# Performance work log

Measured on AMD Instinct MI355X. Metric: run time of the kernel, lower is better.

Reference implementation:

```python
import jax, jax.numpy as jnp
import numpy as np
from jax import lax

CC = 0.25       # commitment cost
EPS_GN = 1e-5   # GroupNorm eps (torch default)


def _conv(x, w, b=None, stride=1, pad=0):
    # x: [B, C, L], w: [O, I, K]
    y = lax.conv_general_dilated(x, w, (stride,), [(pad, pad)],
                                 dimension_numbers=('NCH', 'OIH', 'NCH'))
    if b is not None:
        y = y + b[None, :, None]
    return y


def _convT(x, w, b, pad_lo, pad_hi):
    # stride-2 ConvTranspose1d expressed as lhs-dilated conv; weights kept in
    # equivalent OIW conv form (pad = (k-1-p, k-1-p+output_padding))
    y = lax.conv_general_dilated(x, w, (1,), [(pad_lo, pad_hi)], lhs_dilation=(2,),
                                 dimension_numbers=('NCH', 'OIH', 'NCH'))
    return y + b[None, :, None]


def _gn(x, g, b, groups=8):
    B, C, L = x.shape
    xr = x.reshape(B, groups, C // groups, L)
    m = xr.mean(axis=(2, 3), keepdims=True)
    v = ((xr - m) ** 2).mean(axis=(2, 3), keepdims=True)
    xn = ((xr - m) * lax.rsqrt(v + EPS_GN)).reshape(B, C, L)
    return xn * g[None, :, None] + b[None, :, None]


def _res_block(x, gn1_g, gn1_b, c1_w, gn2_g, gn2_b, c2_w):
    h = jax.nn.relu(_gn(x, gn1_g, gn1_b))
    h = _conv(h, c1_w, None, 1, 1)
    h = jax.nn.relu(_gn(h, gn2_g, gn2_b))
    h = _conv(h, c2_w, None, 1, 0)
    return x + h


def _vq(z, codebook):
    # z: [B, D, L] -> [B, L, D]; eval-mode VQ (no EMA update)
    zin = jnp.transpose(z, (0, 2, 1))
    B, L, D = zin.shape
    flat = zin.reshape(-1, D)
    d = (flat ** 2).sum(1, keepdims=True) + (codebook ** 2).sum(1) - 2.0 * (flat @ codebook.T)
    idx = jnp.argmin(d, axis=1)                       # [B*L]
    q = codebook[idx].reshape(B, L, D)                # gather == onehot @ codebook
    loss = CC * jnp.mean((lax.stop_gradient(q) - zin) ** 2)
    q_st = zin + lax.stop_gradient(q - zin)           # straight-through
    enc = jax.nn.one_hot(idx, codebook.shape[0], dtype=z.dtype)  # [B*L, K]
    avg = enc.mean(0)
    perp = jnp.exp(-jnp.sum(avg * jnp.log(avg + 1e-10)))
    return loss, jnp.transpose(q_st, (0, 2, 1)), perp, enc


def _forward(x, e1_w, e1_b, e2_w, e2_b, e3_w, e3_b,
             r0_gn1_g, r0_gn1_b, r0_c1_w, r0_gn2_g, r0_gn2_b, r0_c2_w,
             r1_gn1_g, r1_gn1_b, r1_c1_w, r1_gn2_g, r1_gn2_b, r1_c2_w,
             pv_w, pv_b, codebook,
             d1_w, d1_b, d2_w, d2_b, d3_w, d3_b,
             bh1_w, bh1_b, bh2_w, bh2_b, bh3_w, bh3_b):
    # encoder: T -> T/4
    h = jax.nn.relu(_conv(x, e1_w, e1_b, 1, 3))
    h = jax.nn.relu(_conv(h, e2_w, e2_b, 2, 2))
    h = _conv(h, e3_w, e3_b, 2, 1)
    h = _res_block(h, r0_gn1_g, r0_gn1_b, r0_c1_w, r0_gn2_g, r0_gn2_b, r0_c2_w)
    h = _res_block(h, r1_gn1_g, r1_gn1_b, r1_c1_w, r1_gn2_g, r1_gn2_b, r1_c2_w)
    z = _conv(h, pv_w, pv_b, 1, 0)  # pre-VQ 1x1 conv; Dropout1d is identity in eval
    loss, quantized, perp, enc = _vq(z, codebook)
    # decoder: T/4 -> T (shapes match exactly; interpolate branches are no-ops)
    d = jax.nn.relu(_convT(quantized, d1_w, d1_b, 1, 2))  # k3 s2 p1 op1
    d = jax.nn.relu(_convT(d, d2_w, d2_b, 2, 3))          # k5 s2 p2 op1
    x_recon = _conv(d, d3_w, d3_b, 1, 3)                  # k7 p3
    z_pooled = quantized.mean(axis=2)                     # [B, D]
    beh = jax.nn.relu(z_pooled @ bh1_w.T + bh1_b)
    beh = jax.nn.relu(beh @ bh2_w.T + bh2_b)              # Dropout eval = identity
    beh = beh @ bh3_w.T + bh3_b
    return loss, x_recon, perp, quantized, enc, beh


def setup_inputs() -> dict:
    key = jax.random.key(0)
    ks = iter(jax.random.split(key, 48))
    def nrm(shape, std=1.0):
        return (std * jax.random.normal(next(ks), shape)).astype(jnp.float32)
    H, RH, D, K, N = 512, 128, 128, 1024, 128
    B, T = 32, 4096
    p = {}
    p['x'] = nrm((B, N, T))
    p['e1_w'] = nrm((H // 4, N, 7), (N * 7) ** -0.5); p['e1_b'] = jnp.zeros((H // 4,), jnp.float32)
    p['e2_w'] = nrm((H // 2, H // 4, 5), (H // 4 * 5) ** -0.5); p['e2_b'] = jnp.zeros((H // 2,), jnp.float32)
    p['e3_w'] = nrm((H, H // 2, 3), (H // 2 * 3) ** -0.5); p['e3_b'] = jnp.zeros((H,), jnp.float32)
    for r in range(2):
        p[f'r{r}_gn1_g'] = jnp.ones((H,), jnp.float32); p[f'r{r}_gn1_b'] = jnp.zeros((H,), jnp.float32)
        p[f'r{r}_c1_w'] = nrm((RH, H, 3), (H * 3) ** -0.5)
        p[f'r{r}_gn2_g'] = jnp.ones((RH,), jnp.float32); p[f'r{r}_gn2_b'] = jnp.zeros((RH,), jnp.float32)
        p[f'r{r}_c2_w'] = nrm((H, RH, 1), RH ** -0.5)
    p['pv_w'] = nrm((D, H, 1), H ** -0.5); p['pv_b'] = jnp.zeros((D,), jnp.float32)
    p['codebook'] = nrm((K, D))  # embedding.weight.data.normal_()
    p['d1_w'] = nrm((H, D, 3), (D * 3) ** -0.5); p['d1_b'] = jnp.zeros((H,), jnp.float32)
    p['d2_w'] = nrm((H // 2, H, 5), (H * 5) ** -0.5); p['d2_b'] = jnp.zeros((H // 2,), jnp.float32)
    p['d3_w'] = nrm((N, H // 2, 7), (H // 2 * 7) ** -0.5); p['d3_b'] = jnp.zeros((N,), jnp.float32)
    p['bh1_w'] = nrm((128, D), D ** -0.5); p['bh1_b'] = jnp.zeros((128,), jnp.float32)
    p['bh2_w'] = nrm((64, 128), 128 ** -0.5); p['bh2_b'] = jnp.zeros((64,), jnp.float32)
    p['bh3_w'] = nrm((4, 64), 64 ** -0.5); p['bh3_b'] = jnp.zeros((4,), jnp.float32)
    return p


def reference(x, e1_w, e1_b, e2_w, e2_b, e3_w, e3_b,
              r0_gn1_g, r0_gn1_b, r0_c1_w, r0_gn2_g, r0_gn2_b, r0_c2_w,
              r1_gn1_g, r1_gn1_b, r1_c1_w, r1_gn2_g, r1_gn2_b, r1_c2_w,
              pv_w, pv_b, codebook,
              d1_w, d1_b, d2_w, d2_b, d3_w, d3_b,
              bh1_w, bh1_b, bh2_w, bh2_b, bh3_w, bh3_b):
    return _forward(x, e1_w, e1_b, e2_w, e2_b, e3_w, e3_b,
                    r0_gn1_g, r0_gn1_b, r0_c1_w, r0_gn2_g, r0_gn2_b, r0_c2_w,
                    r1_gn1_g, r1_gn1_b, r1_c1_w, r1_gn2_g, r1_gn2_b, r1_c2_w,
                    pv_w, pv_b, codebook,
                    d1_w, d1_b, d2_w, d2_b, d3_w, d3_b,
                    bh1_w, bh1_b, bh2_w, bh2_b, bh3_w, bh3_b)
```

## Files before the change

### kernel.cpp

```cpp
#include <hip/hip_runtime.h>


#define SWZ32(j) ((j) + ((((j) >> 5)) << 2))

template<int K, int S, int TT, bool GN, bool RESID, bool RELU_OUT, bool TSTORE, bool VSTORE>
__global__ __launch_bounds__(256, 4) void convtile_k(
    const float* __restrict__ in, const float* __restrict__ w,
    const float* __restrict__ bias, float* __restrict__ out,
    const float* __restrict__ scale, const float* __restrict__ shift,
    const float* __restrict__ resid,
    int Cin, int Lin, int Lout, int pad, int Cout)
{
    constexpr int CI    = (K == 1) ? 32 : 16;
    constexpr int BT    = 16 * TT;
    constexpr int SPAN  = (BT - 1) * S + K;
    constexpr int WN    = (TT - 1) * S + K;
    constexpr int NW4   = (WN + 3) / 4;
    constexpr int JMAX  = 15 * TT * S + 4 * (NW4 - 1);
    constexpr int END1  = SWZ32(JMAX) + 4;
    constexpr int END2  = SWZ32(SPAN - 1) + 1;
    constexpr int SPANP = (((END1 > END2 ? END1 : END2) + 3) & ~3);
    constexpr int LWP   = 68;
    constexpr int PER   = (CI / 4) * K;
    constexpr int NQ    = TT / 4;

    __shared__ float lin[CI * SPANP];
    __shared__ float lw[CI * K * LWP];

    const int tid = threadIdx.x;
    const int tx = tid & 15, ty = tid >> 4;
    const int t0 = blockIdx.x * BT;
    const int o0 = blockIdx.y * 64;
    const int b  = blockIdx.z;

    float acc[4][TT];
    #pragma unroll
    for (int c = 0; c < 4; ++c) {
        float bv = bias ? bias[o0 + 4 * ty + c] : 0.0f;
        #pragma unroll
        for (int u = 0; u < TT; ++u) acc[c][u] = bv;
    }

    int off4[NW4];
    #pragma unroll
    for (int q = 0; q < NW4; ++q) {
        int j = TT * S * tx + 4 * q;
        off4[q] = SWZ32(j);
    }

    const float* inb = in + (size_t)b * Cin * Lin;
    const int p0 = t0 * S - pad;

    constexpr int TPR = 256 / CI;
    const int sci = tid / TPR, sj0 = tid % TPR;
    const int wco = tid >> 2, wpart = tid & 3;
    const int cibase = wpart * (CI / 4);

    for (int ci0 = 0; ci0 < Cin; ci0 += CI) {
        __syncthreads();
        {
            const float* srow = inb + (size_t)(ci0 + sci) * Lin;
            float sc = 0.f, sh = 0.f;
            if (GN) {
                sc = scale[b * Cin + ci0 + sci];
                sh = shift[b * Cin + ci0 + sci];
            }
            for (int j = sj0; j < SPAN; j += TPR) {
                int p = p0 + j;
                bool ok = (p >= 0) && (p < Lin);
                float v = ok ? srow[p] : 0.0f;
                if (GN) v = ok ? fmaxf(v * sc + sh, 0.0f) : 0.0f;
                lin[sci * SPANP + SWZ32(j)] = v;
            }
        }
        {
            const float* wsrc = w + (size_t)(o0 + wco) * Cin * K
                                  + (size_t)ci0 * K + wpart * PER;
            #pragma unroll
            for (int e = 0; e < PER / 4; ++e) {
                const float4 v = *(const float4*)(wsrc + 4 * e);
                #pragma unroll
                for (int i = 0; i < 4; ++i) {
                    const int rem = 4 * e + i;
                    const int cio = rem / K, kk = rem % K;
                    lw[((cibase + cio) * K + kk) * LWP + wco] = ((const float*)&v)[i];
                }
            }
        }
        __syncthreads();

        for (int ci = 0; ci < CI; ++ci) {
            float win[NW4 * 4];
            const float* lrow = &lin[ci * SPANP];
            #pragma unroll
            for (int q = 0; q < NW4; ++q)
                *(float4*)&win[4 * q] = *(const float4*)(lrow + off4[q]);
            #pragma unroll
            for (int k = 0; k < K; ++k) {
                const float4 wv = *(const float4*)&lw[(ci * K + k) * LWP + 4 * ty];
                #pragma unroll
                for (int u = 0; u < TT; ++u) {
                    float x = win[u * S + k];
                    acc[0][u] += x * wv.x;
                    acc[1][u] += x * wv.y;
                    acc[2][u] += x * wv.z;
                    acc[3][u] += x * wv.w;
                }
            }
        }
    }

    if (RESID) {
        #pragma unroll
        for (int c = 0; c < 4; ++c)
            #pragma unroll
            for (int q = 0; q < NQ; ++q) {
                const float4 rv = *(const float4*)(resid +
                    ((size_t)b * Cout + o0 + 4 * ty + c) * Lout + t0 + TT * tx + 4 * q);
                acc[c][4*q+0] += rv.x; acc[c][4*q+1] += rv.y;
                acc[c][4*q+2] += rv.z; acc[c][4*q+3] += rv.w;
            }
    }
    if (RELU_OUT) {
        #pragma unroll
        for (int c = 0; c < 4; ++c)
            #pragma unroll
            for (int u = 0; u < TT; ++u) acc[c][u] = fmaxf(acc[c][u], 0.f);
    }
    if (TSTORE) {
        #pragma unroll
        for (int u = 0; u < TT; ++u) {
            float4 v; v.x = acc[0][u]; v.y = acc[1][u]; v.z = acc[2][u]; v.w = acc[3][u];
            *(float4*)(out + ((size_t)b * Lout + t0 + TT * tx + u) * Cout + o0 + 4 * ty) = v;
        }
    } else if (VSTORE) {
        #pragma unroll
        for (int c = 0; c < 4; ++c)
            #pragma unroll
            for (int q = 0; q < NQ; ++q) {
                float4 v;
                v.x = acc[c][4*q+0]; v.y = acc[c][4*q+1];
                v.z = acc[c][4*q+2]; v.w = acc[c][4*q+3];
                *(float4*)(out + ((size_t)b * Cout + o0 + 4 * ty + c) * Lout
                           + t0 + TT * tx + 4 * q) = v;
            }
    } else {
        #pragma unroll
        for (int c = 0; c < 4; ++c)
            #pragma unroll
            for (int u = 0; u < TT; ++u)
                out[((size_t)b * Cout + o0 + 4 * ty + c) * Lout + t0 + TT * tx + u] = acc[c][u];
    }
}

template<int K, int TT>
__global__ __launch_bounds__(256, 4) void convttile_k(
    const float* __restrict__ in, const float* __restrict__ w,
    const float* __restrict__ bias, float* __restrict__ out,
    int Cin, int Lin, int Cout)
{
    constexpr int CI    = 16;
    constexpr int BT    = 16 * TT;
    constexpr int HALO  = (K == 5) ? 2 : 1;
    constexpr int SPAN  = BT + HALO;
    constexpr int WNl   = TT + HALO;
    constexpr int NW4   = (WNl + 3) / 4;
    constexpr int JMAX  = 15 * TT + 4 * (NW4 - 1);
    constexpr int END1  = SWZ32(JMAX) + 4;
    constexpr int END2  = SWZ32(SPAN - 1) + 1;
    constexpr int SPANP = (((END1 > END2 ? END1 : END2) + 3) & ~3);
    constexpr int LWP   = 68;
    constexpr int PER   = (CI / 4) * K;

    __shared__ float lin[CI * SPANP];
    __shared__ float lw[CI * K * LWP];

    const int tid = threadIdx.x;
    const int tx = tid & 15, ty = tid >> 4;
    const int t20 = blockIdx.x * BT;
    const int o0  = blockIdx.y * 64;
    const int b   = blockIdx.z;
    const int Lout = 2 * Lin;

    float accE[4][TT], accO[4][TT];
    #pragma unroll
    for (int c = 0; c < 4; ++c) {
        float bv = bias[o0 + 4 * ty + c];
        #pragma unroll
        for (int u = 0; u < TT; ++u) { accE[c][u] = bv; accO[c][u] = bv; }
    }

    int off4[NW4];
    #pragma unroll
    for (int q = 0; q < NW4; ++q) {
        int j = TT * tx + 4 * q;
        off4[q] = SWZ32(j);
    }

    const float* inb = in + (size_t)b * Cin * Lin;
    const int p0 = (K == 5) ? (t20 - 1) : t20;

    constexpr int TPR = 256 / CI;
    const int sci = tid / TPR, sj0 = tid % TPR;
    const int wco = tid >> 2, wpart = tid & 3;
    const int cibase = wpart * (CI / 4);

    for (int ci0 = 0; ci0 < Cin; ci0 += CI) {
        __syncthreads();
        {
            const float* srow = inb + (size_t)(ci0 + sci) * Lin;
            for (int j = sj0; j < SPAN; j += TPR) {
                int p = p0 + j;
                bool ok = (p >= 0) && (p < Lin);
                lin[sci * SPANP + SWZ32(j)] = ok ? srow[p] : 0.0f;
            }
        }
        {
            const float* wsrc = w + (size_t)(o0 + wco) * Cin * K
                                  + (size_t)ci0 * K + wpart * PER;
            #pragma unroll
            for (int e = 0; e < PER / 4; ++e) {
                const float4 v = *(const float4*)(wsrc + 4 * e);
                #pragma unroll
                for (int i = 0; i < 4; ++i) {
                    const int rem = 4 * e + i;
                    const int cio = rem / K, kk = rem % K;
                    lw[((cibase + cio) * K + kk) * LWP + wco] = ((const float*)&v)[i];
                }
            }
        }
        __syncthreads();

        for (int ci = 0; ci < CI; ++ci) {
            float win[NW4 * 4];
            const float* lrow = &lin[ci * SPANP];
            #pragma unroll
            for (int q = 0; q < NW4; ++q)
                *(float4*)&win[4 * q] = *(const float4*)(lrow + off4[q]);
            #pragma unroll
            for (int k = 0; k < K; ++k) {
                const float4 wv = *(const float4*)&lw[(ci * K + k) * LWP + 4 * ty];
                const int  joff = (K == 5) ? ((k + 1) >> 1) : (k >> 1);
                const bool toE  = (K == 5) ? ((k & 1) == 0) : (k == 1);
                #pragma unroll
                for (int u = 0; u < TT; ++u) {
                    float x = win[u + joff];
                    if (toE) {
                        accE[0][u] += x * wv.x;
                        accE[1][u] += x * wv.y;
                        accE[2][u] += x * wv.z;
                        accE[3][u] += x * wv.w;
                    } else {
                        accO[0][u] += x * wv.x;
                        accO[1][u] += x * wv.y;
                        accO[2][u] += x * wv.z;
                        accO[3][u] += x * wv.w;
                    }
                }
            }
        }
    }

    size_t base = ((size_t)b * Cout + o0 + 4 * ty) * (size_t)Lout + (size_t)(2 * (t20 + TT * tx));
    #pragma unroll
    for (int c = 0; c < 4; ++c) {
        #pragma unroll
        for (int q = 0; q < TT / 2; ++q) {
            float4 v;
            v.x = fmaxf(accE[c][2*q],   0.f); v.y = fmaxf(accO[c][2*q],   0.f);
            v.z = fmaxf(accE[c][2*q+1], 0.f); v.w = fmaxf(accO[c][2*q+1], 0.f);
            *(float4*)(out + base + (size_t)c * Lout + 4 * q) = v;
        }
    }
}

__global__ __launch_bounds__(256) void gnstats_k(
    const float* __restrict__ x, const float* __restrict__ g,
    const float* __restrict__ be, float* __restrict__ scale,
    float* __restrict__ shift, int C, int L, int G)
{
    int tid = threadIdx.x;
    int b = blockIdx.x / G, gr = blockIdx.x % G;
    int cpg = C / G;
    size_t n = (size_t)cpg * L;
    const float* base = x + ((size_t)b * C + (size_t)gr * cpg) * L;
    float s = 0.f, s2 = 0.f;
    for (size_t idx = tid; idx < n; idx += 256) { float v = base[idx]; s += v; s2 += v * v; }
    __shared__ float rs[256], rq[256];
    rs[tid] = s; rq[tid] = s2; __syncthreads();
    for (int off = 128; off > 0; off >>= 1) {
        if (tid < off) { rs[tid] += rs[tid + off]; rq[tid] += rq[tid + off]; }
        __syncthreads();
    }
    float mean = rs[0] / (float)n;
    float var  = rq[0] / (float)n - mean * mean;
    float inv  = rsqrtf(var + 1e-5f);
    if (tid < cpg) {
        int c = gr * cpg + tid;
        float ga = g[c], bb = be[c];
        scale[b * C + c] = inv * ga;
        shift[b * C + c] = bb - mean * inv * ga;
    }
}

__global__ __launch_bounds__(256) void vq_k(
    const float* __restrict__ z,
    const float* __restrict__ cb,
    float* __restrict__ out_q,
    float* __restrict__ lossAcc,
    unsigned int* __restrict__ hist,
    int* __restrict__ ip_out)
{
    const int tid = threadIdx.x;
    const int pbase = blockIdx.x * 64;
    __shared__ float zs[64 * 129];
    __shared__ float cbs[64 * 129];
    __shared__ float cn[64];
    __shared__ float rd[256];
    __shared__ int   ri[256];
    __shared__ int   ip[64];

    for (int f = tid; f < 64 * 128; f += 256) {
        int p = f >> 7, d = f & 127;
        zs[p * 129 + d] = z[(size_t)pbase * 128 + f];
    }

    float mind[4]; int minc[4];
    #pragma unroll
    for (int a = 0; a < 4; ++a) { mind[a] = 3.4e38f; minc[a] = 0; }
    const int tp = tid >> 4, tr = tid & 15;
    const int prow = tp * 4, crow = tr * 4;

    for (int ct = 0; ct < 16; ++ct) {
        __syncthreads();
        for (int f = tid; f < 64 * 128; f += 256) {
            int c = f >> 7, d = f & 127;
            cbs[c * 129 + d] = cb[((size_t)ct * 64 + c) * 128 + d];
        }
        __syncthreads();
        if (tid < 64) {
            float s = 0.f;
            for (int d = 0; d < 128; ++d) { float v = cbs[tid * 129 + d]; s += v * v; }
            cn[tid] = s;
        }
        __syncthreads();
        float dot[4][4];
        #pragma unroll
        for (int a = 0; a < 4; ++a)
            #pragma unroll
            for (int e = 0; e < 4; ++e) dot[a][e] = 0.f;
        for (int d = 0; d < 128; ++d) {
            float za[4], cc[4];
            #pragma unroll
            for (int a = 0; a < 4; ++a) za[a] = zs[(prow + a) * 129 + d];
            #pragma unroll
            for (int e = 0; e < 4; ++e) cc[e] = cbs[(crow + e) * 129 + d];
            #pragma unroll
            for (int a = 0; a < 4; ++a)
                #pragma unroll
                for (int e = 0; e < 4; ++e) dot[a][e] += za[a] * cc[e];
        }
        #pragma unroll
        for (int e = 0; e < 4; ++e) {
            int c = ct * 64 + crow + e;
            float cne = cn[crow + e];
            #pragma unroll
            for (int a = 0; a < 4; ++a) {
                float dist = cne - 2.0f * dot[a][e];
                if (dist < mind[a]) { mind[a] = dist; minc[a] = c; }
            }
        }
    }

    for (int a = 0; a < 4; ++a) {
        __syncthreads();
        rd[tid] = mind[a]; ri[tid] = minc[a];
        __syncthreads();
        if (tr == 0) {
            float bd = rd[tid]; int bi = ri[tid];
            for (int u = 1; u < 16; ++u) {
                float dv = rd[tid + u]; int iv = ri[tid + u];
                if (dv < bd || (dv == bd && iv < bi)) { bd = dv; bi = iv; }
            }
            ip[prow + a] = bi;
            atomicAdd(&hist[bi], 1u);
        }
    }
    __syncthreads();

    if (tid < 64) ip_out[pbase + tid] = ip[tid];

    float lp = 0.f;
    for (int f = tid; f < 64 * 128; f += 256) {
        int p = f >> 7, d = f & 127;
        int gp = pbase + p, b = gp >> 10, l = gp & 1023;
        float qv = cb[(size_t)ip[p] * 128 + d];
        float zv = zs[p * 129 + d];
        float df = qv - zv; lp += df * df;
        out_q[(((size_t)b * 128 + d) << 10) + l] = qv;
    }
    rd[tid] = lp; __syncthreads();
    for (int off = 128; off > 0; off >>= 1) {
        if (tid < off) rd[tid] += rd[tid + off];
        __syncthreads();
    }
    if (tid == 0) atomicAdd(lossAcc, rd[0]);
}

__global__ __launch_bounds__(256) void enc_k(
    const int* __restrict__ ip, float2* __restrict__ enc)
{
    size_t idx = (size_t)blockIdx.x * 256 + threadIdx.x;
    int p  = (int)(idx >> 9);
    int q2 = (int)(idx & 511);
    int best = ip[p];
    int c0 = q2 * 2;
    float2 v;
    v.x = (c0     == best) ? 1.0f : 0.0f;
    v.y = (c0 + 1 == best) ? 1.0f : 0.0f;
    enc[idx] = v;
}

__global__ __launch_bounds__(256) void pool_k(const float* __restrict__ q, float* __restrict__ zp)
{
    int tid = threadIdx.x;
    const float* row = q + (size_t)blockIdx.x * 1024;
    float s = 0.f;
    for (int l = tid; l < 1024; l += 256) s += row[l];
    __shared__ float rs[256];
    rs[tid] = s; __syncthreads();
    for (int off = 128; off > 0; off >>= 1) {
        if (tid < off) rs[tid] += rs[tid + off];
        __syncthreads();
    }
    if (tid == 0) zp[blockIdx.x] = rs[0] * (1.0f / 1024.0f);
}

__global__ __launch_bounds__(256) void beh_k(
    const float* __restrict__ zp,
    const float* __restrict__ w1, const float* __restrict__ b1,
    const float* __restrict__ w2, const float* __restrict__ b2,
    const float* __restrict__ w3, const float* __restrict__ b3,
    float* __restrict__ out)
{
    __shared__ float zs[32 * 128];
    __shared__ float h1s[32 * 128];
    __shared__ float h2s[32 * 64];
    int tid = threadIdx.x;
    for (int f = tid; f < 4096; f += 256) zs[f] = zp[f];
    __syncthreads();
    for (int f = tid; f < 4096; f += 256) {
        int bi = f >> 7, j = f & 127;
        float acc = b1[j];
        for (int d = 0; d < 128; ++d) acc += zs[bi * 128 + d] * w1[j * 128 + d];
        h1s[f] = fmaxf(acc, 0.f);
    }
    __syncthreads();
    for (int f = tid; f < 2048; f += 256) {
        int bi = f >> 6, j = f & 63;
        float acc = b2[j];
        for (int d = 0; d < 128; ++d) acc += h1s[bi * 128 + d] * w2[j * 128 + d];
        h2s[f] = fmaxf(acc, 0.f);
    }
    __syncthreads();
    if (tid < 128) {
        int bi = tid >> 2, j = tid & 3;
        float acc = b3[j];
        for (int d = 0; d < 64; ++d) acc += h2s[bi * 64 + d] * w3[j * 64 + d];
        out[tid] = acc;
    }
}

__global__ __launch_bounds__(1024) void init_k(unsigned int* hist, float* lossAcc)
{
    hist[threadIdx.x] = 0u;
    if (threadIdx.x == 0) *lossAcc = 0.f;
}

__global__ __launch_bounds__(1024) void fin_k(
    const unsigned int* __restrict__ hist, const float* __restrict__ lossAcc,
    float* __restrict__ out_loss, float* __restrict__ out_perp)
{
    __shared__ float rs[1024];
    int tid = threadIdx.x;
    float avg = (float)hist[tid] * (1.0f / 32768.0f);
    rs[tid] = avg * logf(avg + 1e-10f);
    __syncthreads();
    for (int off = 512; off > 0; off >>= 1) {
        if (tid < off) rs[tid] += rs[tid + off];
        __syncthreads();
    }
    if (tid == 0) {
        out_perp[0] = expf(-rs[0]);
        out_loss[0] = 0.25f * lossAcc[0] * (1.0f / 4194304.0f);
    }
}

extern "C" void kernel_launch(void* const* d_in, const int* in_sizes, int n_in,
                              void* d_out, int out_size, void* d_ws, size_t ws_size,
                              hipStream_t stream)
{
    const float* X    = (const float*)d_in[0];
    const float* e1w  = (const float*)d_in[1];  const float* e1b = (const float*)d_in[2];
    const float* e2w  = (const float*)d_in[3];  const float* e2b = (const float*)d_in[4];
    const float* e3w  = (const float*)d_in[5];  const float* e3b = (const float*)d_in[6];
    const float* r0g1g = (const float*)d_in[7];  const float* r0g1b = (const float*)d_in[8];
    const float* r0c1w = (const float*)d_in[9];
    const float* r0g2g = (const float*)d_in[10]; const float* r0g2b = (const float*)d_in[11];
    const float* r0c2w = (const float*)d_in[12];
    const float* r1g1g = (const float*)d_in[13]; const float* r1g1b = (const float*)d_in[14];
    const float* r1c1w = (const float*)d_in[15];
    const float* r1g2g = (const float*)d_in[16]; const float* r1g2b = (const float*)d_in[17];
    const float* r1c2w = (const float*)d_in[18];
    const float* pvw  = (const float*)d_in[19]; const float* pvb = (const float*)d_in[20];
    const float* CB   = (const float*)d_in[21];
    const float* d1w  = (const float*)d_in[22]; const float* d1b = (const float*)d_in[23];
    const float* d2w  = (const float*)d_in[24]; const float* d2b = (const float*)d_in[25];
    const float* d3w  = (const float*)d_in[26]; const float* d3b = (const float*)d_in[27];
    const float* bh1w = (const float*)d_in[28]; const float* bh1b = (const float*)d_in[29];
    const float* bh2w = (const float*)d_in[30]; const float* bh2b = (const float*)d_in[31];
    const float* bh3w = (const float*)d_in[32]; const float* bh3b = (const float*)d_in[33];

    float* out = (float*)d_out;
    const size_t N_XREC = 16777216ull, N_Q = 4194304ull, N_ENC = 33554432ull;
    float* out_loss = out;
    float* out_xrec = out + 1;
    float* out_perp = out + 1 + N_XREC;
    float* out_q    = out + 2 + N_XREC;
    float* out_enc  = out + 2 + N_XREC + N_Q;
    float* out_beh  = out + 2 + N_XREC + N_Q + N_ENC;

    float* h1 = out + 4;
    float* h3 = h1;
    float* A   = out_enc + 2;
    float* h2  = A;
    float* t2q = A + 16777216;
    float* z   = A + 20971520;
    float* d1o = A;
    float* d2o = A + 16777216;

    float* W = (float*)d_ws;
    float* lossA = W;
    unsigned int* hist = (unsigned int*)(W + 16);
    float* zp   = W + 16 + 1024;
    int* ipArr  = (int*)(W + 16 + 1024 + 4096);
    float* scA  = W + 16 + 1024 + 4096 + 32768;
    float* shA  = scA + 16384;
    float* scB  = shA + 16384;
    float* shB  = scB + 4096;

    init_k<<<dim3(1), dim3(1024), 0, stream>>>(hist, lossA);

    convtile_k<7,1,8,false,false,true,false,true><<<dim3(32, 2, 32), 256, 0, stream>>>(
        X, e1w, e1b, h1, nullptr, nullptr, nullptr, 128, 4096, 4096, 3, 128);
    convtile_k<5,2,4,false,false,true,false,true><<<dim3(32, 4, 32), 256, 0, stream>>>(
        h1, e2w, e2b, h2, nullptr, nullptr, nullptr, 128, 4096, 2048, 2, 256);
    convtile_k<3,2,4,false,false,false,false,true><<<dim3(16, 8, 32), 256, 0, stream>>>(
        h2, e3w, e3b, h3, nullptr, nullptr, nullptr, 256, 2048, 1024, 1, 512);

    gnstats_k<<<dim3(256), 256, 0, stream>>>(h3, r0g1g, r0g1b, scA, shA, 512, 1024, 8);
    convtile_k<3,1,4,true,false,false,false,true><<<dim3(16, 2, 32), 256, 0, stream>>>(
        h3, r0c1w, nullptr, t2q, scA, shA, nullptr, 512, 1024, 1024, 1, 128);
    gnstats_k<<<dim3(256), 256, 0, stream>>>(t2q, r0g2g, r0g2b, scB, shB, 128, 1024, 8);
    convtile_k<1,1,4,true,true,false,false,true><<<dim3(16, 8, 32), 256, 0, stream>>>(
        t2q, r0c2w, nullptr, h3, scB, shB, h3, 128, 1024, 1024, 0, 512);

    gnstats_k<<<dim3(256), 256, 0, stream>>>(h3, r1g1g, r1g1b, scA, shA, 512, 1024, 8);
    convtile_k<3,1,4,true,false,false,false,true><<<dim3(16, 2, 32), 256, 0, stream>>>(
        h3, r1c1w, nullptr, t2q, scA, shA, nullptr, 512, 1024, 1024, 1, 128);
    gnstats_k<<<dim3(256), 256, 0, stream>>>(t2q, r1g2g, r1g2b, scB, shB, 128, 1024, 8);
    convtile_k<1,1,4,true,true,false,false,true><<<dim3(16, 8, 32), 256, 0, stream>>>(
        t2q, r1c2w, nullptr, h3, scB, shB, h3, 128, 1024, 1024, 0, 512);

    convtile_k<1,1,4,false,false,false,true,true><<<dim3(16, 2, 32), 256, 0, stream>>>(
        h3, pvw, pvb, z, nullptr, nullptr, nullptr, 512, 1024, 1024, 0, 128);

    vq_k<<<dim3(512), 256, 0, stream>>>(z, CB, out_q, lossA, hist, ipArr);

    for (int h = 0; h < 2; ++h) {
        convttile_k<3,8><<<dim3(8, 8, 16), 256, 0, stream>>>(
            out_q + (size_t)h * 2097152, d1w, d1b, d1o, 128, 1024, 512);
        convttile_k<5,8><<<dim3(16, 4, 16), 256, 0, stream>>>(
            d1o, d2w, d2b, d2o, 512, 2048, 256);
        convtile_k<7,1,8,false,false,false,false,false><<<dim3(32, 2, 16), 256, 0, stream>>>(
            d2o, d3w, d3b, out_xrec + (size_t)h * 8388608, nullptr, nullptr, nullptr,
            256, 4096, 4096, 3, 128);
    }

    pool_k<<<dim3(4096), 256, 0, stream>>>(out_q, zp);
    beh_k<<<dim3(1), 256, 0, stream>>>(zp, bh1w, bh1b, bh2w, bh2b, bh3w, bh3b, out_beh);

    enc_k<<<dim3(65536), 256, 0, stream>>>(ipArr, (float2*)out_enc);

    fin_k<<<dim3(1), 1024, 0, stream>>>(hist, lossA, out_loss, out_perp);
}
```

Measured before the change: 4.471 ms.

## Register-prefetch next input and weight tiles to overlap loads with compute

In the conv tile kernel, the next channel chunk's input rows (with GroupNorm+ReLU applied) and weights are loaded into registers before the FMA loop of the current chunk, then written to LDS after it. The transposed-conv kernel prefetches only weights this way. Staging reads are also reorganised so each wavefront loads whole rows with 64 lanes. The aim is to hide global memory latency behind compute, at the cost of more registers per thread, which may hurt occupancy under launch_bounds(256,4).

```diff
diff --git a/kernel.cpp b/kernel.cpp
--- a/kernel.cpp
+++ b/kernel.cpp
@@ -23,12 +23,17 @@
     constexpr int LWP   = 68;
     constexpr int PER   = (CI / 4) * K;
     constexpr int NQ    = TT / 4;
+    constexpr int NROWIT = CI / 4;
+    constexpr int NJ     = (SPAN + 63) / 64;
 
     __shared__ float lin[CI * SPANP];
     __shared__ float lw[CI * K * LWP];
 
     const int tid = threadIdx.x;
     const int tx = tid & 15, ty = tid >> 4;
+    const int wvid = tid >> 6, lane = tid & 63;
+    const int wco = tid >> 2, wpart = tid & 3;
+    const int cibase = wpart * (CI / 4);
     const int t0 = blockIdx.x * BT;
     const int o0 = blockIdx.y * 64;
     const int b  = blockIdx.z;
@@ -51,43 +56,61 @@
     const float* inb = in + (size_t)b * Cin * Lin;
     const int p0 = t0 * S - pad;
 
-    constexpr int TPR = 256 / CI;
-    const int sci = tid / TPR, sj0 = tid % TPR;
-    const int wco = tid >> 2, wpart = tid & 3;
-    const int cibase = wpart * (CI / 4);
-
-    for (int ci0 = 0; ci0 < Cin; ci0 += CI) {
-        __syncthreads();
-        {
-            const float* srow = inb + (size_t)(ci0 + sci) * Lin;
+    float  pin[NROWIT][NJ];
+    float4 pw[PER / 4];
+
+    auto prefetch = [&](int ci0) {
+        #pragma unroll
+        for (int it = 0; it < NROWIT; ++it) {
+            const int r = wvid + 4 * it;
+            const float* srow = inb + (size_t)(ci0 + r) * Lin;
             float sc = 0.f, sh = 0.f;
             if (GN) {
-                sc = scale[b * Cin + ci0 + sci];
-                sh = shift[b * Cin + ci0 + sci];
-            }
-            for (int j = sj0; j < SPAN; j += TPR) {
-                int p = p0 + j;
-                bool ok = (p >= 0) && (p < Lin);
+                sc = scale[b * Cin + ci0 + r];
+                sh = shift[b * Cin + ci0 + r];
+            }
+            #pragma unroll
+            for (int jj = 0; jj < NJ; ++jj) {
+                const int j = lane + 64 * jj;
+                const int p = p0 + j;
+                bool ok = (j < SPAN) && (p >= 0) && (p < Lin);
                 float v = ok ? srow[p] : 0.0f;
                 if (GN) v = ok ? fmaxf(v * sc + sh, 0.0f) : 0.0f;
-                lin[sci * SPANP + SWZ32(j)] = v;
-            }
-        }
-        {
-            const float* wsrc = w + (size_t)(o0 + wco) * Cin * K
-                                  + (size_t)ci0 * K + wpart * PER;
-            #pragma unroll
-            for (int e = 0; e < PER / 4; ++e) {
-                const float4 v = *(const float4*)(wsrc + 4 * e);
-                #pragma unroll
-                for (int i = 0; i < 4; ++i) {
-                    const int rem = 4 * e + i;
-                    const int cio = rem / K, kk = rem % K;
-                    lw[((cibase + cio) * K + kk) * LWP + wco] = ((const float*)&v)[i];
-                }
-            }
-        }
-        __syncthreads();
+                pin[it][jj] = v;
+            }
+        }
+        const float* wsrc = w + (size_t)(o0 + wco) * Cin * K
+                              + (size_t)ci0 * K + wpart * PER;
+        #pragma unroll
+        for (int e = 0; e < PER / 4; ++e) pw[e] = *(const float4*)(wsrc + 4 * e);
+    };
+
+    auto write_lds = [&]() {
+        #pragma unroll
+        for (int it = 0; it < NROWIT; ++it) {
+            const int r = wvid + 4 * it;
+            #pragma unroll
+            for (int jj = 0; jj < NJ; ++jj) {
+                const int j = lane + 64 * jj;
+                if (j < SPAN) lin[r * SPANP + SWZ32(j)] = pin[it][jj];
+            }
+        }
+        #pragma unroll
+        for (int e = 0; e < PER / 4; ++e) {
+            #pragma unroll
+            for (int i = 0; i < 4; ++i) {
+                const int rem = 4 * e + i;
+                const int cio = rem / K, kk = rem % K;
+                lw[((cibase + cio) * K + kk) * LWP + wco] = ((const float*)&pw[e])[i];
+            }
+        }
+    };
+
+    prefetch(0);
+    for (int ci0 = 0; ci0 < Cin; ci0 += CI) {
+        write_lds();
+        __syncthreads();
+        if (ci0 + CI < Cin) prefetch(ci0 + CI);
 
         for (int ci = 0; ci < CI; ++ci) {
             float win[NW4 * 4];
@@ -108,6 +131,7 @@
                 }
             }
         }
+        __syncthreads();
     }
 
     if (RESID) {
@@ -171,12 +195,16 @@
     constexpr int SPANP = (((END1 > END2 ? END1 : END2) + 3) & ~3);
     constexpr int LWP   = 68;
     constexpr int PER   = (CI / 4) * K;
+    constexpr int NJ    = (SPAN + 63) / 64;
 
     __shared__ float lin[CI * SPANP];
     __shared__ float lw[CI * K * LWP];
 
     const int tid = threadIdx.x;
     const int tx = tid & 15, ty = tid >> 4;
+    const int wvid = tid >> 6, lane = tid & 63;
+    const int wco = tid >> 2, wpart = tid & 3;
+    const int cibase = wpart * (CI / 4);
     const int t20 = blockIdx.x * BT;
     const int o0  = blockIdx.y * 64;
     const int b   = blockIdx.z;
@@ -200,36 +228,40 @@
     const float* inb = in + (size_t)b * Cin * Lin;
     const int p0 = (K == 5) ? (t20 - 1) : t20;
 
-    constexpr int TPR = 256 / CI;
-    const int sci = tid / TPR, sj0 = tid % TPR;
-    const int wco = tid >> 2, wpart = tid & 3;
-    const int cibase = wpart * (CI / 4);
-
+    float4 pw[PER / 4];
+    auto prefetch_lw = [&](int ci0) {
+        const float* wsrc = w + (size_t)(o0 + wco) * Cin * K
+                              + (size_t)ci0 * K + wpart * PER;
+        #pragma unroll
+        for (int e = 0; e < PER / 4; ++e) pw[e] = *(const float4*)(wsrc + 4 * e);
+    };
+
+    prefetch_lw(0);
     for (int ci0 = 0; ci0 < Cin; ci0 += CI) {
-        __syncthreads();
-        {
-            const float* srow = inb + (size_t)(ci0 + sci) * Lin;
-            for (int j = sj0; j < SPAN; j += TPR) {
-                int p = p0 + j;
-                bool ok = (p >= 0) && (p < Lin);
-                lin[sci * SPANP + SWZ32(j)] = ok ? srow[p] : 0.0f;
-            }
-        }
-        {
-            const float* wsrc = w + (size_t)(o0 + wco) * Cin * K
-                                  + (size_t)ci0 * K + wpart * PER;
-            #pragma unroll
-            for (int e = 0; e < PER / 4; ++e) {
-                const float4 v = *(const float4*)(wsrc + 4 * e);
-                #pragma unroll
-                for (int i = 0; i < 4; ++i) {
-                    const int rem = 4 * e + i;
-                    const int cio = rem / K, kk = rem % K;
-                    lw[((cibase + cio) * K + kk) * LWP + wco] = ((const float*)&v)[i];
-                }
-            }
-        }
-        __syncthreads();
+        #pragma unroll
+        for (int e = 0; e < PER / 4; ++e) {
+            #pragma unroll
+            for (int i = 0; i < 4; ++i) {
+                const int rem = 4 * e + i;
+                const int cio = rem / K, kk = rem % K;
+                lw[((cibase + cio) * K + kk) * LWP + wco] = ((const float*)&pw[e])[i];
+            }
+        }
+        #pragma unroll
+        for (int it = 0; it < CI / 4; ++it) {
+            const int r = wvid + 4 * it;
+            const float* srow = inb + (size_t)(ci0 + r) * Lin;
+            #pragma unroll
+            for (int jj = 0; jj < NJ; ++jj) {
+                const int j = lane + 64 * jj;
+                const int p = p0 + j;
+                bool ok = (j < SPAN) && (p >= 0) && (p < Lin);
+                float v = ok ? srow[p] : 0.0f;
+                if (j < SPAN) lin[r * SPANP + SWZ32(j)] = v;
+            }
+        }
+        __syncthreads();
+        if (ci0 + CI < Cin) prefetch_lw(ci0 + CI);
 
         for (int ci = 0; ci < CI; ++ci) {
             float win[NW4 * 4];
@@ -259,6 +291,7 @@
                 }
             }
         }
+        __syncthreads();
     }
 
     size_t base = ((size_t)b * Cout + o0 + 4 * ty) * (size_t)Lout + (size_t)(2 * (t20 + TT * tx));
```

Result: slower. 4.935 ms (+10.4%).
